# Performance work log

Measured on AMD Instinct MI355X. Metric: run time of the kernel, lower is better.

The kernel has to match this reference:

```python
import jax, jax.numpy as jnp
import numpy as np

F4_E2M1_MAX = 6.0
F8E4M3_MAX = 448.0
E4M3_EPS = 0.015625  # torch.finfo(float8_e4m3fn).tiny = 2**-6
BLOCK = 16
KE2M1 = jnp.array([0.0, 0.5, 1.0, 1.5, 2.0, 3.0, 4.0, 6.0], dtype=jnp.float32)


def round_to_e4m3(x):
    # emulate cast to float8_e4m3fn and back (round-to-nearest-even)
    return x.astype(jnp.float8_e4m3fn).astype(jnp.float32)


def fp4_121_positive(x):
    step1 = jnp.round(2.0 * x) / 2.0   # subnormal-ish region [0,2): step 0.5
    step2 = jnp.round(x)               # [2,4): step 1
    step3 = 2.0 * jnp.round(x / 2.0)   # [4,6]: step 2
    return jnp.where(x < 2.0, step1, jnp.where(x < 4.0, step2, step3))


def cast_to_fp4(x):
    return jnp.sign(x) * fp4_121_positive(jnp.abs(x))


def unpack_fp4_from_uint8(a, m, n):
    # a: int-typed tensor holding byte values in [0,256); two fp4 codes per byte
    high = (a.reshape(-1) >> 4) & 0xF
    low = a.reshape(-1) & 0xF
    combined = jnp.stack((low, high), axis=1).reshape(m, n)  # interleave low,high
    signs = (combined & 8) != 0
    abs_idx = combined & 7
    return KE2M1[abs_idx] * jnp.where(signs, -1.0, 1.0)


def dequant_nvfp4_packed(data_lp, out_scales, per_tensor_scale):
    m, half_n = data_lp.shape
    n = half_n * 2
    data_hp = unpack_fp4_from_uint8(data_lp, m, n)           # [m, n] float32
    scale_fp = out_scales / per_tensor_scale                  # [m, n/16]
    data_hp = data_hp.reshape(m, -1, BLOCK) * scale_fp.reshape(m, -1, 1)
    return data_hp.reshape(m, n)


def qdq_nvfp4(x):
    m, n = x.shape
    tensor_amax = jnp.max(jnp.abs(x))
    pts = jnp.clip(tensor_amax / F8E4M3_MAX, E4M3_EPS, F8E4M3_MAX)  # per-tensor scale
    xb = x.reshape(m, -1, BLOCK)
    block_scale = jnp.max(jnp.abs(xb), axis=-1) / F4_E2M1_MAX       # [m, n/16]
    scaled_bs = round_to_e4m3(jnp.clip(block_scale / pts, E4M3_EPS, F8E4M3_MAX))
    total_scale = pts * scaled_bs                                   # [m, n/16]
    data_scaled = jnp.clip(xb / total_scale[..., None], -F4_E2M1_MAX, F4_E2M1_MAX)
    data_lp = cast_to_fp4(data_scaled)                              # unpacked fp4 values
    # dequant: out_scales / (1/pts) == scaled_bs * pts == total_scale
    return (data_lp * total_scale[..., None]).reshape(m, n)


def setup_inputs() -> dict:
    key = jax.random.key(0)
    k1, k2, k3 = jax.random.split(key, 3)
    M, K, N = 16384, 2048, 2048  # tokens, in_features, out_features
    x = jax.random.normal(k1, (M, K), dtype=jnp.float32)
    weight_packed = jax.random.randint(k2, (N, K // 2), 0, 256, dtype=jnp.int32)
    # fp8-representable positive block scales
    weight_scale = round_to_e4m3(jax.random.uniform(k3, (N, K // 16), dtype=jnp.float32,
                                                    minval=0.05, maxval=1.0))
    weight_global_scale = jnp.ones((1,), dtype=jnp.float32)
    return {"x": x, "weight_packed": weight_packed,
            "weight_scale": weight_scale, "weight_global_scale": weight_global_scale}


def reference(x, weight_packed, weight_scale, weight_global_scale):
    hp_weight = dequant_nvfp4_packed(weight_packed, weight_scale, weight_global_scale)
    x_dq = qdq_nvfp4(x)
    return x_dq @ hp_weight.T
```

## Files before the change

kernel.cpp:

```cpp
#include <hip/hip_runtime.h>

typedef unsigned short u16;
typedef unsigned int u32;
typedef __attribute__((ext_vector_type(8))) short short8;
typedef __attribute__((ext_vector_type(4))) float floatx4;

static constexpr int M = 16384, N = 2048, K = 2048;


__device__ inline u16 f32_to_bf16(float x) {
    u32 u = __float_as_uint(x);
    u += 0x7FFFu + ((u >> 16) & 1u);
    return (u16)(u >> 16);
}

__device__ inline float e4m3_rne(float x) {
    u32 u = __float_as_uint(x);
    u += 0x7FFFFu + ((u >> 20) & 1u);
    u &= 0xFFF00000u;
    return __uint_as_float(u);
}

__device__ inline float fp4_dec(u32 c) {
    u32 e = (c >> 1) & 3u;
    float m = (float)(c & 1u);
    float v = e ? (2.0f + m) * (float)(1u << e) * 0.25f : 0.5f * m;
    return (c & 8u) ? -v : v;
}

__device__ inline float fp4_round_mag(float a) {
    if (a < 2.0f) return rintf(2.0f * a) * 0.5f;
    if (a < 4.0f) return rintf(a);
    return 2.0f * rintf(a * 0.5f);
}

__device__ inline float pts_from_amax(float amax) {
    return fminf(fmaxf(amax / 448.0f, 0.015625f), 448.0f);
}


__global__ void amax_part(const float4* __restrict__ x, float* __restrict__ part, int n4) {
    int idx = blockIdx.x * blockDim.x + threadIdx.x;
    int stride = gridDim.x * blockDim.x;
    float m = 0.0f;
    for (int i = idx; i < n4; i += stride) {
        float4 v = x[i];
        m = fmaxf(m, fmaxf(fmaxf(fabsf(v.x), fabsf(v.y)), fmaxf(fabsf(v.z), fabsf(v.w))));
    }
#pragma unroll
    for (int off = 32; off > 0; off >>= 1)
        m = fmaxf(m, __shfl_down(m, off));
    __shared__ float sm[4];
    if ((threadIdx.x & 63) == 0) sm[threadIdx.x >> 6] = m;
    __syncthreads();
    if (threadIdx.x == 0)
        part[blockIdx.x] = fmaxf(fmaxf(sm[0], sm[1]), fmaxf(sm[2], sm[3]));
}


__global__ void amax_fin(const float* __restrict__ part, u32* __restrict__ out) {
    int t = threadIdx.x;
    float m = fmaxf(part[t], part[t + 1024]);
#pragma unroll
    for (int off = 32; off > 0; off >>= 1)
        m = fmaxf(m, __shfl_down(m, off));
    __shared__ float sm[16];
    if ((t & 63) == 0) sm[t >> 6] = m;
    __syncthreads();
    if (t < 16) {
        m = sm[t];
#pragma unroll
        for (int off = 8; off > 0; off >>= 1)
            m = fmaxf(m, __shfl_down(m, off));
        if (t == 0) *out = __float_as_uint(m);
    }
}


__global__ void quant_x(const float4* __restrict__ x, uint2* __restrict__ aq,
                        const u32* __restrict__ amax_bits, int nvec) {
    int idx = blockIdx.x * blockDim.x + threadIdx.x;
    if (idx >= nvec) return;
    float4 v = x[idx];

    float bm = fmaxf(fmaxf(fabsf(v.x), fabsf(v.y)), fmaxf(fabsf(v.z), fabsf(v.w)));
    bm = fmaxf(bm, __shfl_xor(bm, 1));
    bm = fmaxf(bm, __shfl_xor(bm, 2));

    float pts = pts_from_amax(__uint_as_float(*amax_bits));
    float bs = bm / 6.0f;
    float sbs = e4m3_rne(fminf(fmaxf(bs / pts, 0.015625f), 448.0f));
    float ts = pts * sbs;

    float vf[4] = {v.x, v.y, v.z, v.w};
    u16 o[4];
#pragma unroll
    for (int i = 0; i < 4; i++) {
        float s = vf[i] / ts;
        s = fminf(fmaxf(s, -6.0f), 6.0f);
        float lp = copysignf(fp4_round_mag(fabsf(s)), s);
        o[i] = f32_to_bf16(lp * sbs);
    }
    aq[idx] = *(const uint2*)o;
}


__global__ void dequant_w(const int* __restrict__ wp, const float* __restrict__ wsc,
                          const float* __restrict__ wgs, u16* __restrict__ wq, int total) {
    int idx = blockIdx.x * blockDim.x + threadIdx.x;
    if (idx >= total) return;
    constexpr int Khalf = K / 2;
    int n = idx >> 10;
    int kb = idx & (Khalf - 1);
    u32 byte = (u32)wp[idx] & 0xFFu;
    float scale = wsc[(size_t)n * (K / 16) + (kb >> 3)] / wgs[0];
    float lo = fp4_dec(byte & 0xFu) * scale;
    float hi = fp4_dec((byte >> 4) & 0xFu) * scale;
    u32 out = (u32)f32_to_bf16(lo) | ((u32)f32_to_bf16(hi) << 16);
    ((u32*)wq)[idx] = out;
}


#define GLDS(g, l)                                                              \
    __builtin_amdgcn_global_load_lds(                                           \
        (const __attribute__((address_space(1))) unsigned int*)(g),             \
        (__attribute__((address_space(3))) unsigned int*)(l), 16, 0, 0)

__global__ __launch_bounds__(256, 3) void gemm_bt(
    const u16* __restrict__ A, const u16* __restrict__ B,
    float* __restrict__ C, const u32* __restrict__ amax_bits)
{
    __shared__ u16 lA[128 * 32];
    __shared__ u16 lB[128 * 32];

    const int tid = threadIdx.x;
    const int w = tid >> 6, lane = tid & 63;

    const int id = blockIdx.x;
    const int xcd = id & 7;
    const int local = id >> 3;
    const int bm = xcd * 16 + (local >> 4);
    const int bn = local & 15;

    const int wm = w >> 1, wn = w & 1;
    const int r = lane & 15, q = lane >> 4;

    floatx4 acc[4][4] = {};

    const int srow = lane >> 2;
    const int scol = (lane & 3) * 8;
    const u16* gA0 = A + (size_t)(bm * 128 + w * 32 + srow) * K + scol;
    const u16* gA1 = gA0 + (size_t)16 * K;
    const u16* gB0 = B + (size_t)(bn * 128 + w * 32 + srow) * K + scol;
    const u16* gB1 = gB0 + (size_t)16 * K;
    u16* lA0 = &lA[(w * 32) * 32];
    u16* lA1 = &lA[(w * 32 + 16) * 32];
    u16* lB0 = &lB[(w * 32) * 32];
    u16* lB1 = &lB[(w * 32 + 16) * 32];

    for (int kt = 0; kt < K; kt += 32) {
        GLDS(gA0 + kt, lA0);
        GLDS(gA1 + kt, lA1);
        GLDS(gB0 + kt, lB0);
        GLDS(gB1 + kt, lB1);
        __syncthreads();

        short8 af[4], bf[4];
#pragma unroll
        for (int i = 0; i < 4; i++)
            af[i] = *(const short8*)&lA[(wm * 64 + i * 16 + r) * 32 + q * 8];
#pragma unroll
        for (int j = 0; j < 4; j++)
            bf[j] = *(const short8*)&lB[(wn * 64 + j * 16 + r) * 32 + q * 8];

#pragma unroll
        for (int i = 0; i < 4; i++)
#pragma unroll
            for (int j = 0; j < 4; j++)
                acc[i][j] = __builtin_amdgcn_mfma_f32_16x16x32_bf16(
                    af[i], bf[j], acc[i][j], 0, 0, 0);

        __syncthreads();
    }

    float pts = pts_from_amax(__uint_as_float(*amax_bits));

    float* Cb = C + (size_t)(bm * 128 + wm * 64 + q * 4) * N + bn * 128 + wn * 64 + r;
#pragma unroll
    for (int i = 0; i < 4; i++)
#pragma unroll
        for (int j = 0; j < 4; j++)
#pragma unroll
            for (int t = 0; t < 4; t++)
                Cb[(size_t)(i * 16 + t) * N + j * 16] = pts * acc[i][j][t];
}


extern "C" void kernel_launch(void* const* d_in, const int* in_sizes, int n_in,
                              void* d_out, int out_size, void* d_ws, size_t ws_size,
                              hipStream_t stream) {
    const float* x   = (const float*)d_in[0];
    const int*   wp  = (const int*)d_in[1];
    const float* wsc = (const float*)d_in[2];
    const float* wgs = (const float*)d_in[3];
    float* out = (float*)d_out;

    u32*   amax_ws = (u32*)d_ws;
    float* part    = (float*)((char*)d_ws + 64);
    u16*   aq      = (u16*)((char*)d_ws + 16384);
    u16*   wq      = aq + (size_t)M * K;

    amax_part<<<2048, 256, 0, stream>>>((const float4*)x, part, M * K / 4);
    amax_fin<<<1, 1024, 0, stream>>>(part, amax_ws);
    quant_x<<<(M * K / 4) / 256, 256, 0, stream>>>((const float4*)x, (uint2*)aq,
                                                   amax_ws, M * K / 4);
    dequant_w<<<(N * (K / 2)) / 256, 256, 0, stream>>>(wp, wsc, wgs, wq, N * (K / 2));
    gemm_bt<<<(M / 128) * (N / 128), 256, 0, stream>>>(aq, wq, out, amax_ws);
}
```

Baseline: 413.2 us.

## Merge quant/dequant kernels and double GEMM K-step per barrier

Combines the activation quantization and weight dequantization into a single launch that dispatches on block index, removing one kernel launch and its tail. The GEMM now loads two 32-wide K slices into separate LDS buffers per iteration and runs both MFMA groups between a single pair of barriers, halving the number of synchronizations and issuing more loads in flight. This doubles LDS use per block (32 KB), which may reduce occupancy against the 3-blocks launch bound.

```diff
diff --git a/kernel.cpp b/kernel.cpp
--- a/kernel.cpp
+++ b/kernel.cpp
@@ -77,47 +77,48 @@
 }
 
 
-__global__ void quant_x(const float4* __restrict__ x, uint2* __restrict__ aq,
-                        const u32* __restrict__ amax_bits, int nvec) {
-    int idx = blockIdx.x * blockDim.x + threadIdx.x;
-    if (idx >= nvec) return;
-    float4 v = x[idx];
-
-    float bm = fmaxf(fmaxf(fabsf(v.x), fabsf(v.y)), fmaxf(fabsf(v.z), fabsf(v.w)));
-    bm = fmaxf(bm, __shfl_xor(bm, 1));
-    bm = fmaxf(bm, __shfl_xor(bm, 2));
-
-    float pts = pts_from_amax(__uint_as_float(*amax_bits));
-    float bs = bm / 6.0f;
-    float sbs = e4m3_rne(fminf(fmaxf(bs / pts, 0.015625f), 448.0f));
-    float ts = pts * sbs;
-
-    float vf[4] = {v.x, v.y, v.z, v.w};
-    u16 o[4];
-#pragma unroll
-    for (int i = 0; i < 4; i++) {
-        float s = vf[i] / ts;
-        s = fminf(fmaxf(s, -6.0f), 6.0f);
-        float lp = copysignf(fp4_round_mag(fabsf(s)), s);
-        o[i] = f32_to_bf16(lp * sbs);
-    }
-    aq[idx] = *(const uint2*)o;
-}
-
-
-__global__ void dequant_w(const int* __restrict__ wp, const float* __restrict__ wsc,
-                          const float* __restrict__ wgs, u16* __restrict__ wq, int total) {
-    int idx = blockIdx.x * blockDim.x + threadIdx.x;
-    if (idx >= total) return;
-    constexpr int Khalf = K / 2;
-    int n = idx >> 10;
-    int kb = idx & (Khalf - 1);
-    u32 byte = (u32)wp[idx] & 0xFFu;
-    float scale = wsc[(size_t)n * (K / 16) + (kb >> 3)] / wgs[0];
-    float lo = fp4_dec(byte & 0xFu) * scale;
-    float hi = fp4_dec((byte >> 4) & 0xFu) * scale;
-    u32 out = (u32)f32_to_bf16(lo) | ((u32)f32_to_bf16(hi) << 16);
-    ((u32*)wq)[idx] = out;
+static constexpr int QB = (M * K / 4) / 256;
+static constexpr int DB = (N * (K / 2)) / 256;
+
+__global__ void prep(const float4* __restrict__ x, uint2* __restrict__ aq,
+                     const u32* __restrict__ amax_bits,
+                     const int* __restrict__ wp, const float* __restrict__ wsc,
+                     const float* __restrict__ wgs, u16* __restrict__ wq) {
+    if (blockIdx.x < QB) {
+        int idx = blockIdx.x * blockDim.x + threadIdx.x;
+        float4 v = x[idx];
+
+        float bm = fmaxf(fmaxf(fabsf(v.x), fabsf(v.y)), fmaxf(fabsf(v.z), fabsf(v.w)));
+        bm = fmaxf(bm, __shfl_xor(bm, 1));
+        bm = fmaxf(bm, __shfl_xor(bm, 2));
+
+        float pts = pts_from_amax(__uint_as_float(*amax_bits));
+        float bs = bm / 6.0f;
+        float sbs = e4m3_rne(fminf(fmaxf(bs / pts, 0.015625f), 448.0f));
+        float ts = pts * sbs;
+
+        float vf[4] = {v.x, v.y, v.z, v.w};
+        u16 o[4];
+#pragma unroll
+        for (int i = 0; i < 4; i++) {
+            float s = vf[i] / ts;
+            s = fminf(fmaxf(s, -6.0f), 6.0f);
+            float lp = copysignf(fp4_round_mag(fabsf(s)), s);
+            o[i] = f32_to_bf16(lp * sbs);
+        }
+        aq[idx] = *(const uint2*)o;
+    } else {
+        int idx = (blockIdx.x - QB) * blockDim.x + threadIdx.x;
+        constexpr int Khalf = K / 2;
+        int n = idx >> 10;
+        int kb = idx & (Khalf - 1);
+        u32 byte = (u32)wp[idx] & 0xFFu;
+        float scale = wsc[(size_t)n * (K / 16) + (kb >> 3)] / wgs[0];
+        float lo = fp4_dec(byte & 0xFu) * scale;
+        float hi = fp4_dec((byte >> 4) & 0xFu) * scale;
+        u32 out = (u32)f32_to_bf16(lo) | ((u32)f32_to_bf16(hi) << 16);
+        ((u32*)wq)[idx] = out;
+    }
 }
 
 
@@ -130,8 +131,8 @@
     const u16* __restrict__ A, const u16* __restrict__ B,
     float* __restrict__ C, const u32* __restrict__ amax_bits)
 {
-    __shared__ u16 lA[128 * 32];
-    __shared__ u16 lB[128 * 32];
+    __shared__ u16 lA[2][128 * 32];
+    __shared__ u16 lB[2][128 * 32];
 
     const int tid = threadIdx.x;
     const int w = tid >> 6, lane = tid & 63;
@@ -153,32 +154,43 @@
     const u16* gA1 = gA0 + (size_t)16 * K;
     const u16* gB0 = B + (size_t)(bn * 128 + w * 32 + srow) * K + scol;
     const u16* gB1 = gB0 + (size_t)16 * K;
-    u16* lA0 = &lA[(w * 32) * 32];
-    u16* lA1 = &lA[(w * 32 + 16) * 32];
-    u16* lB0 = &lB[(w * 32) * 32];
-    u16* lB1 = &lB[(w * 32 + 16) * 32];
-
-    for (int kt = 0; kt < K; kt += 32) {
-        GLDS(gA0 + kt, lA0);
-        GLDS(gA1 + kt, lA1);
-        GLDS(gB0 + kt, lB0);
-        GLDS(gB1 + kt, lB1);
+    u16* dA[2][2], * dB[2][2];
+#pragma unroll
+    for (int h = 0; h < 2; h++) {
+        dA[h][0] = &lA[h][(w * 32) * 32];
+        dA[h][1] = &lA[h][(w * 32 + 16) * 32];
+        dB[h][0] = &lB[h][(w * 32) * 32];
+        dB[h][1] = &lB[h][(w * 32 + 16) * 32];
+    }
+
+    for (int kt = 0; kt < K; kt += 64) {
+        GLDS(gA0 + kt,      dA[0][0]);
+        GLDS(gA1 + kt,      dA[0][1]);
+        GLDS(gA0 + kt + 32, dA[1][0]);
+        GLDS(gA1 + kt + 32, dA[1][1]);
+        GLDS(gB0 + kt,      dB[0][0]);
+        GLDS(gB1 + kt,      dB[0][1]);
+        GLDS(gB0 + kt + 32, dB[1][0]);
+        GLDS(gB1 + kt + 32, dB[1][1]);
         __syncthreads();
 
-        short8 af[4], bf[4];
-#pragma unroll
-        for (int i = 0; i < 4; i++)
-            af[i] = *(const short8*)&lA[(wm * 64 + i * 16 + r) * 32 + q * 8];
-#pragma unroll
-        for (int j = 0; j < 4; j++)
-            bf[j] = *(const short8*)&lB[(wn * 64 + j * 16 + r) * 32 + q * 8];
-
-#pragma unroll
-        for (int i = 0; i < 4; i++)
+#pragma unroll
+        for (int h = 0; h < 2; h++) {
+            short8 af[4], bf[4];
+#pragma unroll
+            for (int i = 0; i < 4; i++)
+                af[i] = *(const short8*)&lA[h][(wm * 64 + i * 16 + r) * 32 + q * 8];
 #pragma unroll
             for (int j = 0; j < 4; j++)
-                acc[i][j] = __builtin_amdgcn_mfma_f32_16x16x32_bf16(
-                    af[i], bf[j], acc[i][j], 0, 0, 0);
+                bf[j] = *(const short8*)&lB[h][(wn * 64 + j * 16 + r) * 32 + q * 8];
+
+#pragma unroll
+            for (int i = 0; i < 4; i++)
+#pragma unroll
+                for (int j = 0; j < 4; j++)
+                    acc[i][j] = __builtin_amdgcn_mfma_f32_16x16x32_bf16(
+                        af[i], bf[j], acc[i][j], 0, 0, 0);
+        }
 
         __syncthreads();
     }
@@ -212,8 +224,7 @@
 
     amax_part<<<2048, 256, 0, stream>>>((const float4*)x, part, M * K / 4);
     amax_fin<<<1, 1024, 0, stream>>>(part, amax_ws);
-    quant_x<<<(M * K / 4) / 256, 256, 0, stream>>>((const float4*)x, (uint2*)aq,
-                                                   amax_ws, M * K / 4);
-    dequant_w<<<(N * (K / 2)) / 256, 256, 0, stream>>>(wp, wsc, wgs, wq, N * (K / 2));
+    prep<<<QB + DB, 256, 0, stream>>>((const float4*)x, (uint2*)aq, amax_ws,
+                                      wp, wsc, wgs, wq);
     gemm_bt<<<(M / 128) * (N / 128), 256, 0, stream>>>(aq, wq, out, amax_ws);
 }
```

Result: no change. 409.3 us (-0.9%).

## Switch GEMM to 32x32x16 MFMA tiles and merge quant/dequant into one kernel

Applied to the files above, without the earlier changes.

The GEMM inner loop now uses 32x32x16 bf16 MFMA with 2x2 accumulator tiles per wave instead of 4x4 16x16x32 tiles. This halves the number of MFMA issues and changes the LDS fragment read pattern and the output store mapping. Launch bounds rise to 4 waves per SIMD to allow more occupancy. The activation quantisation and weight dequantisation kernels are fused into a single launch, which saves one kernel launch. The trade-off is higher register pressure from 16-wide accumulators under the tighter launch bound, and possible LDS bank conflicts with the new access pattern.

```diff
diff --git a/kernel.cpp b/kernel.cpp
--- a/kernel.cpp
+++ b/kernel.cpp
@@ -3,7 +3,7 @@
 typedef unsigned short u16;
 typedef unsigned int u32;
 typedef __attribute__((ext_vector_type(8))) short short8;
-typedef __attribute__((ext_vector_type(4))) float floatx4;
+typedef __attribute__((ext_vector_type(16))) float floatx16;
 
 static constexpr int M = 16384, N = 2048, K = 2048;
 
@@ -77,47 +77,48 @@
 }
 
 
-__global__ void quant_x(const float4* __restrict__ x, uint2* __restrict__ aq,
-                        const u32* __restrict__ amax_bits, int nvec) {
-    int idx = blockIdx.x * blockDim.x + threadIdx.x;
-    if (idx >= nvec) return;
-    float4 v = x[idx];
-
-    float bm = fmaxf(fmaxf(fabsf(v.x), fabsf(v.y)), fmaxf(fabsf(v.z), fabsf(v.w)));
-    bm = fmaxf(bm, __shfl_xor(bm, 1));
-    bm = fmaxf(bm, __shfl_xor(bm, 2));
-
-    float pts = pts_from_amax(__uint_as_float(*amax_bits));
-    float bs = bm / 6.0f;
-    float sbs = e4m3_rne(fminf(fmaxf(bs / pts, 0.015625f), 448.0f));
-    float ts = pts * sbs;
-
-    float vf[4] = {v.x, v.y, v.z, v.w};
-    u16 o[4];
-#pragma unroll
-    for (int i = 0; i < 4; i++) {
-        float s = vf[i] / ts;
-        s = fminf(fmaxf(s, -6.0f), 6.0f);
-        float lp = copysignf(fp4_round_mag(fabsf(s)), s);
-        o[i] = f32_to_bf16(lp * sbs);
-    }
-    aq[idx] = *(const uint2*)o;
-}
-
-
-__global__ void dequant_w(const int* __restrict__ wp, const float* __restrict__ wsc,
-                          const float* __restrict__ wgs, u16* __restrict__ wq, int total) {
-    int idx = blockIdx.x * blockDim.x + threadIdx.x;
-    if (idx >= total) return;
-    constexpr int Khalf = K / 2;
-    int n = idx >> 10;
-    int kb = idx & (Khalf - 1);
-    u32 byte = (u32)wp[idx] & 0xFFu;
-    float scale = wsc[(size_t)n * (K / 16) + (kb >> 3)] / wgs[0];
-    float lo = fp4_dec(byte & 0xFu) * scale;
-    float hi = fp4_dec((byte >> 4) & 0xFu) * scale;
-    u32 out = (u32)f32_to_bf16(lo) | ((u32)f32_to_bf16(hi) << 16);
-    ((u32*)wq)[idx] = out;
+static constexpr int QB = (M * K / 4) / 256;
+static constexpr int DB = (N * (K / 2)) / 256;
+
+__global__ void prep(const float4* __restrict__ x, uint2* __restrict__ aq,
+                     const u32* __restrict__ amax_bits,
+                     const int* __restrict__ wp, const float* __restrict__ wsc,
+                     const float* __restrict__ wgs, u16* __restrict__ wq) {
+    if (blockIdx.x < QB) {
+        int idx = blockIdx.x * blockDim.x + threadIdx.x;
+        float4 v = x[idx];
+
+        float bm = fmaxf(fmaxf(fabsf(v.x), fabsf(v.y)), fmaxf(fabsf(v.z), fabsf(v.w)));
+        bm = fmaxf(bm, __shfl_xor(bm, 1));
+        bm = fmaxf(bm, __shfl_xor(bm, 2));
+
+        float pts = pts_from_amax(__uint_as_float(*amax_bits));
+        float bs = bm / 6.0f;
+        float sbs = e4m3_rne(fminf(fmaxf(bs / pts, 0.015625f), 448.0f));
+        float ts = pts * sbs;
+
+        float vf[4] = {v.x, v.y, v.z, v.w};
+        u16 o[4];
+#pragma unroll
+        for (int i = 0; i < 4; i++) {
+            float s = vf[i] / ts;
+            s = fminf(fmaxf(s, -6.0f), 6.0f);
+            float lp = copysignf(fp4_round_mag(fabsf(s)), s);
+            o[i] = f32_to_bf16(lp * sbs);
+        }
+        aq[idx] = *(const uint2*)o;
+    } else {
+        int idx = (blockIdx.x - QB) * blockDim.x + threadIdx.x;
+        constexpr int Khalf = K / 2;
+        int n = idx >> 10;
+        int kb = idx & (Khalf - 1);
+        u32 byte = (u32)wp[idx] & 0xFFu;
+        float scale = wsc[(size_t)n * (K / 16) + (kb >> 3)] / wgs[0];
+        float lo = fp4_dec(byte & 0xFu) * scale;
+        float hi = fp4_dec((byte >> 4) & 0xFu) * scale;
+        u32 out = (u32)f32_to_bf16(lo) | ((u32)f32_to_bf16(hi) << 16);
+        ((u32*)wq)[idx] = out;
+    }
 }
 
 
@@ -126,7 +127,7 @@
         (const __attribute__((address_space(1))) unsigned int*)(g),             \
         (__attribute__((address_space(3))) unsigned int*)(l), 16, 0, 0)
 
-__global__ __launch_bounds__(256, 3) void gemm_bt(
+__global__ __launch_bounds__(256, 4) void gemm_bt(
     const u16* __restrict__ A, const u16* __restrict__ B,
     float* __restrict__ C, const u32* __restrict__ amax_bits)
 {
@@ -143,9 +144,10 @@
     const int bn = local & 15;
 
     const int wm = w >> 1, wn = w & 1;
-    const int r = lane & 15, q = lane >> 4;
-
-    floatx4 acc[4][4] = {};
+    const int ml = lane & 31;
+    const int kg = lane >> 5;
+
+    floatx16 acc[2][2] = {};
 
     const int srow = lane >> 2;
     const int scol = (lane & 3) * 8;
@@ -165,34 +167,39 @@
         GLDS(gB1 + kt, lB1);
         __syncthreads();
 
-        short8 af[4], bf[4];
-#pragma unroll
-        for (int i = 0; i < 4; i++)
-            af[i] = *(const short8*)&lA[(wm * 64 + i * 16 + r) * 32 + q * 8];
-#pragma unroll
-        for (int j = 0; j < 4; j++)
-            bf[j] = *(const short8*)&lB[(wn * 64 + j * 16 + r) * 32 + q * 8];
-
-#pragma unroll
-        for (int i = 0; i < 4; i++)
-#pragma unroll
-            for (int j = 0; j < 4; j++)
-                acc[i][j] = __builtin_amdgcn_mfma_f32_16x16x32_bf16(
-                    af[i], bf[j], acc[i][j], 0, 0, 0);
+        short8 af[2][2], bf[2][2];
+#pragma unroll
+        for (int h = 0; h < 2; h++)
+#pragma unroll
+            for (int i = 0; i < 2; i++) {
+                af[h][i] = *(const short8*)&lA[(wm * 64 + i * 32 + ml) * 32 + h * 16 + kg * 8];
+                bf[h][i] = *(const short8*)&lB[(wn * 64 + i * 32 + ml) * 32 + h * 16 + kg * 8];
+            }
+
+#pragma unroll
+        for (int h = 0; h < 2; h++)
+#pragma unroll
+            for (int i = 0; i < 2; i++)
+#pragma unroll
+                for (int j = 0; j < 2; j++)
+                    acc[i][j] = __builtin_amdgcn_mfma_f32_32x32x16_bf16(
+                        af[h][i], bf[h][j], acc[i][j], 0, 0, 0);
 
         __syncthreads();
     }
 
     float pts = pts_from_amax(__uint_as_float(*amax_bits));
 
-    float* Cb = C + (size_t)(bm * 128 + wm * 64 + q * 4) * N + bn * 128 + wn * 64 + r;
-#pragma unroll
-    for (int i = 0; i < 4; i++)
-#pragma unroll
-        for (int j = 0; j < 4; j++)
-#pragma unroll
-            for (int t = 0; t < 4; t++)
-                Cb[(size_t)(i * 16 + t) * N + j * 16] = pts * acc[i][j][t];
+    float* Cb = C + (size_t)(bm * 128 + wm * 64) * N + bn * 128 + wn * 64;
+#pragma unroll
+    for (int i = 0; i < 2; i++)
+#pragma unroll
+        for (int j = 0; j < 2; j++)
+#pragma unroll
+            for (int t = 0; t < 16; t++) {
+                int row = i * 32 + (t & 3) + 8 * (t >> 2) + 4 * kg;
+                Cb[(size_t)row * N + j * 32 + ml] = pts * acc[i][j][t];
+            }
 }
 
 
@@ -212,8 +219,7 @@
 
     amax_part<<<2048, 256, 0, stream>>>((const float4*)x, part, M * K / 4);
     amax_fin<<<1, 1024, 0, stream>>>(part, amax_ws);
-    quant_x<<<(M * K / 4) / 256, 256, 0, stream>>>((const float4*)x, (uint2*)aq,
-                                                   amax_ws, M * K / 4);
-    dequant_w<<<(N * (K / 2)) / 256, 256, 0, stream>>>(wp, wsc, wgs, wq, N * (K / 2));
+    prep<<<QB + DB, 256, 0, stream>>>((const float4*)x, (uint2*)aq, amax_ws,
+                                      wp, wsc, wgs, wq);
     gemm_bt<<<(M / 128) * (N / 128), 256, 0, stream>>>(aq, wq, out, amax_ws);
 }
```

Result: no change. 420.5 us (+1.8%).
